# Kernel optimization log

Hardware: AMD Instinct MI355X
Metric: run time of the kernel (lower is better)

The kernel has to match this reference:

```python
import jax, jax.numpy as jnp
import numpy as np

H = 128          # num_hidden
NUM_IN = 256     # 2*H: h_E (H) + gathered neighbor h_V (H)
SCALE = 30.0
LN_EPS = 1e-5


def _ln(x, g, b):
    mu = jnp.mean(x, axis=-1, keepdims=True)
    var = jnp.mean((x - mu) ** 2, axis=-1, keepdims=True)
    return (x - mu) * jax.lax.rsqrt(var + LN_EPS) * g + b


def _gather_nodes(nodes, idx):
    # nodes: [B,L,C], idx: [B,L,K] -> [B,L,K,C]
    B = nodes.shape[0]
    return nodes[jnp.arange(B)[:, None, None], idx]


def _mlp3(x, W1, b1, W2, b2, W3, b3):
    h = jax.nn.gelu(x @ W1 + b1, approximate=False)
    h = jax.nn.gelu(h @ W2 + b2, approximate=False)
    return h @ W3 + b3


def setup_inputs() -> dict:
    key = jax.random.key(0)
    ks = jax.random.split(key, 16)
    B, L, K = 2, 2048, 48
    s = 0.02
    inp = {
        "h_V": jax.random.normal(ks[0], (B, L, H), jnp.float32),
        "h_E": jax.random.normal(ks[1], (B, L, K, H), jnp.float32),
        "E_idx": jax.random.randint(ks[2], (B, L, K), 0, L, jnp.int32),
        "mask_V": jnp.ones((B, L), jnp.float32),
        "mask_attend": jnp.ones((B, L, K), jnp.float32),
        # node-update MLP
        "W1": jax.random.normal(ks[3], (H + NUM_IN, H), jnp.float32) * s,
        "b1": jnp.zeros((H,), jnp.float32),
        "W2": jax.random.normal(ks[4], (H, H), jnp.float32) * s,
        "b2": jnp.zeros((H,), jnp.float32),
        "W3": jax.random.normal(ks[5], (H, H), jnp.float32) * s,
        "b3": jnp.zeros((H,), jnp.float32),
        # edge-update MLP
        "W11": jax.random.normal(ks[6], (H + NUM_IN, H), jnp.float32) * s,
        "b11": jnp.zeros((H,), jnp.float32),
        "W12": jax.random.normal(ks[7], (H, H), jnp.float32) * s,
        "b12": jnp.zeros((H,), jnp.float32),
        "W13": jax.random.normal(ks[8], (H, H), jnp.float32) * s,
        "b13": jnp.zeros((H,), jnp.float32),
        # position-wise FFN (H -> 4H -> H)
        "Win": jax.random.normal(ks[9], (H, 4 * H), jnp.float32) * s,
        "bin": jnp.zeros((4 * H,), jnp.float32),
        "Wout": jax.random.normal(ks[10], (4 * H, H), jnp.float32) * s,
        "bout": jnp.zeros((H,), jnp.float32),
        # LayerNorms
        "g1": jnp.ones((H,), jnp.float32), "be1": jnp.zeros((H,), jnp.float32),
        "g2": jnp.ones((H,), jnp.float32), "be2": jnp.zeros((H,), jnp.float32),
        "g3": jnp.ones((H,), jnp.float32), "be3": jnp.zeros((H,), jnp.float32),
    }
    return inp


def reference(h_V, h_E, E_idx, mask_V, mask_attend,
              W1, b1, W2, b2, W3, b3,
              W11, b11, W12, b12, W13, b13,
              Win, bin, Wout, bout,
              g1, be1, g2, be2, g3, be3):
    K = h_E.shape[-2]
    # --- node update: gather, concat, 3-layer MLP, masked mean-sum, LN residual ---
    h_nbr = _gather_nodes(h_V, E_idx)                               # [B,L,K,H]
    h_V_exp = jnp.broadcast_to(h_V[:, :, None, :], h_nbr.shape)     # [B,L,K,H]
    h_EV = jnp.concatenate([h_V_exp, h_E, h_nbr], axis=-1)          # [B,L,K,3H]
    h_msg = _mlp3(h_EV, W1, b1, W2, b2, W3, b3)                     # [B,L,K,H]
    h_msg = mask_attend[..., None] * h_msg
    dh = jnp.sum(h_msg, axis=-2) / SCALE                            # [B,L,H]
    h_V = _ln(h_V + dh, g1, be1)
    # position-wise FFN + LN residual
    dh = jax.nn.gelu(h_V @ Win + bin, approximate=False) @ Wout + bout
    h_V = _ln(h_V + dh, g2, be2)
    h_V = mask_V[..., None] * h_V
    # --- edge update ---
    h_nbr = _gather_nodes(h_V, E_idx)
    h_V_exp = jnp.broadcast_to(h_V[:, :, None, :], h_nbr.shape)
    h_EV = jnp.concatenate([h_V_exp, h_E, h_nbr], axis=-1)
    h_msg = _mlp3(h_EV, W11, b11, W12, b12, W13, b13)
    h_E = _ln(h_E + h_msg, g3, be3)
    return (h_V, h_E)
```

## Files before the change

kernel.cpp:

```cpp
#include <hip/hip_runtime.h>
#include <hip/hip_bf16.h>

typedef __attribute__((ext_vector_type(8))) short short8;
typedef __attribute__((ext_vector_type(4))) float f32x4;

__device__ inline short f2bf(float f) {
    unsigned u = __builtin_bit_cast(unsigned, f);
    u += 0x7fffu + ((u >> 16) & 1u);
    return (short)(u >> 16);
}
__device__ inline float bf2f(short s) {
    return __builtin_bit_cast(float, ((unsigned)(unsigned short)s) << 16);
}
__device__ inline unsigned cvt_pk_bf16(float a, float b) {
    unsigned r;
    asm("v_cvt_pk_bf16_f32 %0, %1, %2" : "=v"(r) : "v"(a), "v"(b));
    return r;
}
__device__ inline float gelu_fast(float x) {
    float z = x * (1.0f + 0.044715f * x * x);
    float e = __expf(1.5957691216f * z);
    return x - x * __builtin_amdgcn_rcpf(e + 1.0f);
}
__device__ inline float wred(float s) {
#pragma unroll
    for (int o = 32; o; o >>= 1) s += __shfl_xor(s, o, 64);
    return s;
}

__global__ void pack_all_kernel(const float* __restrict__ W1, const float* __restrict__ W2,
                                const float* __restrict__ W3, const float* __restrict__ W11,
                                const float* __restrict__ W12, const float* __restrict__ W13,
                                const float* __restrict__ Win, const float* __restrict__ Wout,
                                short* __restrict__ out) {
    int b = blockIdx.x;
    if (b < 80) {
        int which = b >> 3;
        const float* Ws[10] = {W1 + 128 * 128, W2, W3, W11 + 128 * 128, W12, W13,
                               W1, W1 + 256 * 128, W11, W11 + 256 * 128};
        const float* W = Ws[which];
        int i = (b & 7) * 256 + threadIdx.x;
        int lane = i & 63, tile = i >> 6;
        int kt = tile & 3, nt = tile >> 2;
        int n = nt * 16 + (lane & 15);
        int k0 = kt * 32 + (lane >> 4) * 8;
        short8 v;
#pragma unroll
        for (int j = 0; j < 8; ++j) v[j] = f2bf(W[(size_t)(k0 + j) * 128 + n]);
        *(short8*)(out + (size_t)which * 16384 + (size_t)i * 8) = v;
    } else if (b < 112) {
        int i = (b - 80) * 256 + threadIdx.x;
        int lane = i & 63, tile = i >> 6;
        int kt = tile & 3, nt = tile >> 2;
        int n = nt * 16 + (lane & 15);
        int k0 = kt * 32 + (lane >> 4) * 8;
        short8 v;
#pragma unroll
        for (int j = 0; j < 8; ++j) v[j] = f2bf(Win[(size_t)(k0 + j) * 512 + n]);
        *(short8*)(out + 163840 + (size_t)i * 8) = v;
    } else {
        int i = (b - 112) * 256 + threadIdx.x;
        int lane = i & 63, tile = i >> 6;
        int kt = tile & 15, nt = tile >> 4;
        int n = nt * 16 + (lane & 15);
        int k0 = kt * 32 + (lane >> 4) * 8;
        short8 v;
#pragma unroll
        for (int j = 0; j < 8; ++j) v[j] = f2bf(Wout[(size_t)(k0 + j) * 128 + n]);
        *(short8*)(out + 229376 + (size_t)i * 8) = v;
    }
}

__global__ __launch_bounds__(256) void node_pre_kernel(
    const float* __restrict__ hV, const short8* __restrict__ Bs,
    const short8* __restrict__ Bn, const float* __restrict__ bias,
    float* __restrict__ Ys, short* __restrict__ Yn) {
    int n0 = blockIdx.x * 16;
    int tid = threadIdx.x, lane = tid & 63, w = tid >> 6;
    __shared__ __align__(16) short A_sw[16 * 128];
    {
        int off = tid * 8;
        int r = off >> 7, c0 = off & 127;
        const float* src = hV + (size_t)n0 * 128 + off;
        float4 f0 = *(const float4*)(src);
        float4 f1 = *(const float4*)(src + 4);
        uint4 u;
        u.x = cvt_pk_bf16(f0.x, f0.y); u.y = cvt_pk_bf16(f0.z, f0.w);
        u.z = cvt_pk_bf16(f1.x, f1.y); u.w = cvt_pk_bf16(f1.z, f1.w);
        *(uint4*)((char*)A_sw + r * 256 + ((c0 * 2) ^ ((r & 7) << 4))) = u;
    }
    __syncthreads();
    const short8* Bp = (w < 2) ? Bs : Bn;
    f32x4 acc[4];
#pragma unroll
    for (int n2 = 0; n2 < 4; ++n2) acc[n2] = (f32x4){0.f, 0.f, 0.f, 0.f};
#pragma unroll
    for (int kt = 0; kt < 4; ++kt) {
        int row = lane & 15;
        int kb = (kt * 32 + (lane >> 4) * 8) * 2;
        short8 a = *(const short8*)((const char*)A_sw + row * 256 + (kb ^ ((row & 7) << 4)));
#pragma unroll
        for (int n2 = 0; n2 < 4; ++n2) {
            int ntl = (w & 1) * 4 + n2;
            short8 bf = Bp[(ntl * 4 + kt) * 64 + lane];
            acc[n2] = __builtin_amdgcn_mfma_f32_16x16x32_bf16(a, bf, acc[n2], 0, 0, 0);
        }
    }
    if (w < 2) {
#pragma unroll
        for (int n2 = 0; n2 < 4; ++n2) {
            int col = ((w & 1) * 4 + n2) * 16 + (lane & 15);
            float bv = bias[col];
#pragma unroll
            for (int i = 0; i < 4; ++i) {
                int row = (lane >> 4) * 4 + i;
                Ys[(size_t)(n0 + row) * 128 + col] = acc[n2][i] + bv;
            }
        }
    } else {
#pragma unroll
        for (int n2 = 0; n2 < 4; ++n2) {
            int col = ((w & 1) * 4 + n2) * 16 + (lane & 15);
#pragma unroll
            for (int i = 0; i < 4; ++i) {
                int row = (lane >> 4) * 4 + i;
                Yn[(size_t)(n0 + row) * 128 + col] = f2bf(acc[n2][i]);
            }
        }
    }
}


__device__ inline void gemm48_a(const short* A_sw, const short8* __restrict__ Wp,
                                int w, int lane, f32x4 acc[3][2]) {
#pragma unroll
    for (int mt = 0; mt < 3; ++mt)
#pragma unroll
        for (int n2 = 0; n2 < 2; ++n2) acc[mt][n2] = (f32x4){0.f, 0.f, 0.f, 0.f};
#pragma unroll
    for (int kt = 0; kt < 4; ++kt) {
        short8 a[3];
        int kb = (kt * 32 + (lane >> 4) * 8) * 2;
#pragma unroll
        for (int mt = 0; mt < 3; ++mt) {
            int row = mt * 16 + (lane & 15);
            a[mt] = *(const short8*)((const char*)A_sw + row * 256 + (kb ^ ((row & 7) << 4)));
        }
#pragma unroll
        for (int n2 = 0; n2 < 2; ++n2) {
            short8 bf = Wp[((w * 2 + n2) * 4 + kt) * 64 + lane];
#pragma unroll
            for (int mt = 0; mt < 3; ++mt)
                acc[mt][n2] = __builtin_amdgcn_mfma_f32_16x16x32_bf16(a[mt], bf, acc[mt][n2], 0, 0, 0);
        }
    }
}

__device__ inline void gemm48_swz(const short* A_sw, const short8* __restrict__ Wp,
                                  int w, int lane, f32x4 acc[2][3]) {
#pragma unroll
    for (int m2 = 0; m2 < 2; ++m2)
#pragma unroll
        for (int nt = 0; nt < 3; ++nt) acc[m2][nt] = (f32x4){0.f, 0.f, 0.f, 0.f};
#pragma unroll
    for (int kt = 0; kt < 4; ++kt) {
        int kb = (kt * 32 + (lane >> 4) * 8) * 2;
        short8 e[3];
#pragma unroll
        for (int nt = 0; nt < 3; ++nt) {
            int row = nt * 16 + (lane & 15);
            e[nt] = *(const short8*)((const char*)A_sw + row * 256 + (kb ^ ((row & 7) << 4)));
        }
#pragma unroll
        for (int m2 = 0; m2 < 2; ++m2) {
            short8 wf = Wp[((w * 2 + m2) * 4 + kt) * 64 + lane];
#pragma unroll
            for (int nt = 0; nt < 3; ++nt)
                acc[m2][nt] = __builtin_amdgcn_mfma_f32_16x16x32_bf16(wf, e[nt], acc[m2][nt], 0, 0, 0);
        }
    }
}

__device__ inline void stage_hE(const float* __restrict__ Eb, short* A_sw, int tid) {
#pragma unroll
    for (int i = 0; i < 3; ++i) {
        int e = tid + i * 256;
        int r = e >> 4, c0 = (e & 15) * 8;
        float4 f0 = *(const float4*)(Eb + r * 128 + c0);
        float4 f1 = *(const float4*)(Eb + r * 128 + c0 + 4);
        uint4 u;
        u.x = cvt_pk_bf16(f0.x, f0.y); u.y = cvt_pk_bf16(f0.z, f0.w);
        u.z = cvt_pk_bf16(f1.x, f1.y); u.w = cvt_pk_bf16(f1.z, f1.w);
        *(uint4*)((char*)A_sw + r * 256 + ((c0 * 2) ^ ((r & 7) << 4))) = u;
    }
}

__device__ inline void gather_Yn(const short* __restrict__ Yng, const int* __restrict__ Eidx,
                                 int node, int bb, int tid, short* Ygb) {
    if (tid < 192) {
        int r = tid >> 2, q = tid & 3;
        int idx = Eidx[node * 48 + r];
        const short8* src = (const short8*)(Yng + ((size_t)bb * 2048 + idx) * 128 + q * 32);
        short8* dst = (short8*)(Ygb + r * 136 + q * 32);
        dst[0] = src[0];
        dst[1] = src[1];
        dst[2] = src[2];
        dst[3] = src[3];
    }
}

__device__ inline void epi_l1(f32x4 acc[2][3], const float* Ysh, const short* Ygb,
                              short* A_sw, int w, int lane) {
#pragma unroll
    for (int m2 = 0; m2 < 2; ++m2) {
        int featb = (w * 2 + m2) * 16 + ((lane >> 4) << 2);
        float ys0 = Ysh[featb], ys1 = Ysh[featb + 1];
        float ys2 = Ysh[featb + 2], ys3 = Ysh[featb + 3];
#pragma unroll
        for (int nt = 0; nt < 3; ++nt) {
            int edge = nt * 16 + (lane & 15);
            uint2 yv = *(const uint2*)(Ygb + edge * 136 + featb);
            float v0 = gelu_fast(acc[m2][nt][0] + ys0 + __builtin_bit_cast(float, yv.x << 16));
            float v1 = gelu_fast(acc[m2][nt][1] + ys1 + __builtin_bit_cast(float, yv.x & 0xffff0000u));
            float v2 = gelu_fast(acc[m2][nt][2] + ys2 + __builtin_bit_cast(float, yv.y << 16));
            float v3 = gelu_fast(acc[m2][nt][3] + ys3 + __builtin_bit_cast(float, yv.y & 0xffff0000u));
            uint2 pk = {cvt_pk_bf16(v0, v1), cvt_pk_bf16(v2, v3)};
            *(uint2*)((char*)A_sw + edge * 256 + ((featb * 2) ^ ((edge & 7) << 4))) = pk;
        }
    }
}

__device__ inline void epi_l2(f32x4 acc[2][3], const float* __restrict__ b,
                              short* A_sw, int w, int lane) {
#pragma unroll
    for (int m2 = 0; m2 < 2; ++m2) {
        int featb = (w * 2 + m2) * 16 + ((lane >> 4) << 2);
        float b0 = b[featb], b1 = b[featb + 1], b2v = b[featb + 2], b3v = b[featb + 3];
#pragma unroll
        for (int nt = 0; nt < 3; ++nt) {
            int edge = nt * 16 + (lane & 15);
            float v0 = gelu_fast(acc[m2][nt][0] + b0);
            float v1 = gelu_fast(acc[m2][nt][1] + b1);
            float v2 = gelu_fast(acc[m2][nt][2] + b2v);
            float v3 = gelu_fast(acc[m2][nt][3] + b3v);
            uint2 pk = {cvt_pk_bf16(v0, v1), cvt_pk_bf16(v2, v3)};
            *(uint2*)((char*)A_sw + edge * 256 + ((featb * 2) ^ ((edge & 7) << 4))) = pk;
        }
    }
}

__global__ __launch_bounds__(256) void node_msg_kernel(
    const float* __restrict__ hV, const float* __restrict__ hE,
    const int* __restrict__ Eidx, const float* __restrict__ maskAtt,
    const short8* __restrict__ W1bp, const short8* __restrict__ W2p,
    const short8* __restrict__ W3p, const float* __restrict__ b2,
    const float* __restrict__ b3, const float* __restrict__ Ysg,
    const short* __restrict__ Yng, const float* __restrict__ g1,
    const float* __restrict__ be1, float* __restrict__ hv1out) {
    const int node = blockIdx.x;
    const int bb = node >> 11;
    const int tid = threadIdx.x;
    const int lane = tid & 63, w = tid >> 6;

    __shared__ __align__(16) short A_sw[48 * 128];
    __shared__ __align__(16) short Ygb[48 * 136];
    __shared__ float Ysh[128];
    __shared__ float mask_s[48];
    __shared__ float red[8];

    stage_hE(hE + (size_t)node * 6144, A_sw, tid);
    if (tid < 128) Ysh[tid] = Ysg[(size_t)node * 128 + tid];
    if (tid >= 128 && tid < 176) mask_s[tid - 128] = maskAtt[node * 48 + tid - 128];
    gather_Yn(Yng, Eidx, node, bb, tid, Ygb);
    __syncthreads();

    f32x4 acc[2][3];
    gemm48_swz(A_sw, W1bp, w, lane, acc);
    __syncthreads();
    epi_l1(acc, Ysh, Ygb, A_sw, w, lane);
    __syncthreads();
    gemm48_swz(A_sw, W2p, w, lane, acc);
    __syncthreads();
    epi_l2(acc, b2, A_sw, w, lane);
    __syncthreads();

    f32x4 acc3[3][2];
    gemm48_a(A_sw, W3p, w, lane, acc3);
    float u[2];
#pragma unroll
    for (int n2 = 0; n2 < 2; ++n2) {
        int col = (w * 2 + n2) * 16 + (lane & 15);
        float b3c = b3[col];
        float s = 0.f;
#pragma unroll
        for (int mt = 0; mt < 3; ++mt)
#pragma unroll
            for (int i = 0; i < 4; ++i) {
                int row = mt * 16 + (lane >> 4) * 4 + i;
                s += (acc3[mt][n2][i] + b3c) * mask_s[row];
            }
        s += __shfl_xor(s, 16, 64);
        s += __shfl_xor(s, 32, 64);
        u[n2] = hV[(size_t)node * 128 + col] + s * (1.0f / 30.0f);
    }
    float ps = wred(u[0] + u[1]) * 0.25f;
    float pq = wred(u[0] * u[0] + u[1] * u[1]) * 0.25f;
    if (lane == 0) { red[w] = ps; red[4 + w] = pq; }
    __syncthreads();
    float S = red[0] + red[1] + red[2] + red[3];
    float Q = red[4] + red[5] + red[6] + red[7];
    float mu = S * (1.0f / 128.0f);
    float var = Q * (1.0f / 128.0f) - mu * mu;
    float rs = rsqrtf(var + 1e-5f);
    if ((lane >> 4) == 0) {
#pragma unroll
        for (int n2 = 0; n2 < 2; ++n2) {
            int col = (w * 2 + n2) * 16 + (lane & 15);
            hv1out[(size_t)node * 128 + col] = (u[n2] - mu) * rs * g1[col] + be1[col];
        }
    }
}

__global__ __launch_bounds__(256) void ffn_kernel(
    const float* __restrict__ hv1, const short8* __restrict__ Winp,
    const float* __restrict__ binp, const short8* __restrict__ Woutp,
    const float* __restrict__ bout, const float* __restrict__ g2,
    const float* __restrict__ be2, const float* __restrict__ maskV,
    float* __restrict__ hVout) {
    int n0 = blockIdx.x * 16;
    int tid = threadIdx.x, lane = tid & 63, w = tid >> 6;
    __shared__ float X[16 * 128];
    __shared__ __align__(16) short A_sw[16 * 128];
    __shared__ __align__(16) short H_sw[16 * 512];

    {
        int off = tid * 8;
        int r = off >> 7, c0 = off & 127;
        const float* src = hv1 + (size_t)n0 * 128 + off;
        float4 f0 = *(const float4*)(src);
        float4 f1 = *(const float4*)(src + 4);
        *(float4*)(&X[off]) = f0;
        *(float4*)(&X[off + 4]) = f1;
        uint4 u;
        u.x = cvt_pk_bf16(f0.x, f0.y); u.y = cvt_pk_bf16(f0.z, f0.w);
        u.z = cvt_pk_bf16(f1.x, f1.y); u.w = cvt_pk_bf16(f1.z, f1.w);
        *(uint4*)((char*)A_sw + r * 256 + ((c0 * 2) ^ ((r & 7) << 4))) = u;
    }
    __syncthreads();

    f32x4 acc1[8];
#pragma unroll
    for (int n2 = 0; n2 < 8; ++n2) acc1[n2] = (f32x4){0.f, 0.f, 0.f, 0.f};
#pragma unroll
    for (int kt = 0; kt < 4; ++kt) {
        int row = lane & 15;
        int kb = (kt * 32 + (lane >> 4) * 8) * 2;
        short8 a = *(const short8*)((const char*)A_sw + row * 256 + (kb ^ ((row & 7) << 4)));
#pragma unroll
        for (int n2 = 0; n2 < 8; ++n2) {
            short8 bf = Winp[((w * 8 + n2) * 4 + kt) * 64 + lane];
            acc1[n2] = __builtin_amdgcn_mfma_f32_16x16x32_bf16(a, bf, acc1[n2], 0, 0, 0);
        }
    }
#pragma unroll
    for (int n2 = 0; n2 < 8; ++n2) {
        int col = (w * 8 + n2) * 16 + (lane & 15);
        float bv = binp[col];
#pragma unroll
        for (int i = 0; i < 4; ++i) {
            int row = (lane >> 4) * 4 + i;
            float v = gelu_fast(acc1[n2][i] + bv);
            *(short*)((char*)H_sw + row * 1024 + ((col * 2) ^ ((row & 7) << 4))) = f2bf(v);
        }
    }
    __syncthreads();

    f32x4 acc2[2];
    acc2[0] = (f32x4){0.f, 0.f, 0.f, 0.f};
    acc2[1] = (f32x4){0.f, 0.f, 0.f, 0.f};
#pragma unroll
    for (int kt = 0; kt < 16; ++kt) {
        int row = lane & 15;
        int kb = (kt * 32 + (lane >> 4) * 8) * 2;
        short8 a = *(const short8*)((const char*)H_sw + row * 1024 + (kb ^ ((row & 7) << 4)));
#pragma unroll
        for (int n2 = 0; n2 < 2; ++n2) {
            short8 bf = Woutp[((w * 2 + n2) * 16 + kt) * 64 + lane];
            acc2[n2] = __builtin_amdgcn_mfma_f32_16x16x32_bf16(a, bf, acc2[n2], 0, 0, 0);
        }
    }
#pragma unroll
    for (int n2 = 0; n2 < 2; ++n2) {
        int col = (w * 2 + n2) * 16 + (lane & 15);
        float bo = bout[col];
#pragma unroll
        for (int i = 0; i < 4; ++i) {
            int row = (lane >> 4) * 4 + i;
            X[row * 128 + col] += acc2[n2][i] + bo;
        }
    }
    __syncthreads();

#pragma unroll
    for (int p = 0; p < 4; ++p) {
        int r = p * 4 + w;
        float u0 = X[r * 128 + lane], u1 = X[r * 128 + lane + 64];
        float s = wred(u0 + u1);
        float q = wred(u0 * u0 + u1 * u1);
        float mu = s * (1.0f / 128.0f);
        float var = q * (1.0f / 128.0f) - mu * mu;
        float rs = rsqrtf(var + 1e-5f);
        float mv = maskV[n0 + r];
        hVout[(size_t)(n0 + r) * 128 + lane] = mv * ((u0 - mu) * rs * g2[lane] + be2[lane]);
        hVout[(size_t)(n0 + r) * 128 + lane + 64] = mv * ((u1 - mu) * rs * g2[lane + 64] + be2[lane + 64]);
    }
}

__global__ __launch_bounds__(256) void edge_upd_kernel(
    const float* __restrict__ hE, const int* __restrict__ Eidx,
    const short8* __restrict__ W11bp, const short8* __restrict__ W12p,
    const short8* __restrict__ W13p, const float* __restrict__ b12,
    const float* __restrict__ b13, const float* __restrict__ Ysg,
    const short* __restrict__ Yng, const float* __restrict__ g3,
    const float* __restrict__ be3, float* __restrict__ hEout) {
    const int node = blockIdx.x;
    const int bb = node >> 11;
    const int tid = threadIdx.x;
    const int lane = tid & 63, w = tid >> 6;

    __shared__ __align__(16) short A_sw[48 * 128];
    __shared__ __align__(16) short Ygb[48 * 136];
    __shared__ float Ysh[128];

    const float* Eb = hE + (size_t)node * 6144;
    stage_hE(Eb, A_sw, tid);
    if (tid < 128) Ysh[tid] = Ysg[(size_t)node * 128 + tid];
    gather_Yn(Yng, Eidx, node, bb, tid, Ygb);
    __syncthreads();

    f32x4 acc[2][3];
    gemm48_swz(A_sw, W11bp, w, lane, acc);
    __syncthreads();
    epi_l1(acc, Ysh, Ygb, A_sw, w, lane);
    __syncthreads();
    gemm48_swz(A_sw, W12p, w, lane, acc);
    __syncthreads();
    epi_l2(acc, b12, A_sw, w, lane);
    __syncthreads();

    f32x4 acc3[3][2];
    gemm48_a(A_sw, W13p, w, lane, acc3);
#pragma unroll
    for (int mt = 0; mt < 3; ++mt)
#pragma unroll
        for (int n2 = 0; n2 < 2; ++n2) {
            int col = (w * 2 + n2) * 16 + (lane & 15);
            float bv = b13[col];
#pragma unroll
            for (int i = 0; i < 4; ++i) {
                int row = mt * 16 + (lane >> 4) * 4 + i;
                float v = acc3[mt][n2][i] + bv + Eb[row * 128 + col];
                Ygb[row * 136 + col] = f2bf(v);
            }
        }
    __syncthreads();

    float* outb = hEout + (size_t)node * 6144;
    float gl0 = g3[lane], gl1 = g3[lane + 64];
    float bl0 = be3[lane], bl1 = be3[lane + 64];
#pragma unroll
    for (int p = 0; p < 12; ++p) {
        int r = p * 4 + w;
        float u0 = bf2f(Ygb[r * 136 + lane]);
        float u1 = bf2f(Ygb[r * 136 + lane + 64]);
        float s = wred(u0 + u1);
        float q = wred(u0 * u0 + u1 * u1);
        float mu = s * (1.0f / 128.0f);
        float var = q * (1.0f / 128.0f) - mu * mu;
        float rs = rsqrtf(var + 1e-5f);
        outb[r * 128 + lane] = (u0 - mu) * rs * gl0 + bl0;
        outb[r * 128 + lane + 64] = (u1 - mu) * rs * gl1 + bl1;
    }
}

extern "C" void kernel_launch(void* const* d_in, const int* in_sizes, int n_in,
                              void* d_out, int out_size, void* d_ws, size_t ws_size,
                              hipStream_t stream) {
    const float* hV      = (const float*)d_in[0];
    const float* hE      = (const float*)d_in[1];
    const int*   Eidx    = (const int*)d_in[2];
    const float* maskV   = (const float*)d_in[3];
    const float* maskAtt = (const float*)d_in[4];
    const float* W1  = (const float*)d_in[5];
    const float* b1  = (const float*)d_in[6];
    const float* W2  = (const float*)d_in[7];
    const float* b2  = (const float*)d_in[8];
    const float* W3  = (const float*)d_in[9];
    const float* b3  = (const float*)d_in[10];
    const float* W11 = (const float*)d_in[11];
    const float* b11 = (const float*)d_in[12];
    const float* W12 = (const float*)d_in[13];
    const float* b12 = (const float*)d_in[14];
    const float* W13 = (const float*)d_in[15];
    const float* b13 = (const float*)d_in[16];
    const float* Win = (const float*)d_in[17];
    const float* binp= (const float*)d_in[18];
    const float* Wout= (const float*)d_in[19];
    const float* bout= (const float*)d_in[20];
    const float* g1  = (const float*)d_in[21];
    const float* be1 = (const float*)d_in[22];
    const float* g2  = (const float*)d_in[23];
    const float* be2 = (const float*)d_in[24];
    const float* g3  = (const float*)d_in[25];
    const float* be3 = (const float*)d_in[26];

    char* ws = (char*)d_ws;
    short* Wpk  = (short*)ws;
    float* Ys   = (float*)(ws + 1048576);
    short* Yn   = (short*)(ws + 1048576 + 2097152);
    float* hv1  = (float*)(ws + 1048576 + 2097152 + 1048576);

    float* hVout = (float*)d_out;
    float* hEout = hVout + 2 * 2048 * 128;

    const int NNODE = 2 * 2048;

    pack_all_kernel<<<144, 256, 0, stream>>>(W1, W2, W3, W11, W12, W13, Win, Wout, Wpk);

    node_pre_kernel<<<NNODE / 16, 256, 0, stream>>>(hV,
        (const short8*)(Wpk + 98304), (const short8*)(Wpk + 114688), b1, Ys, Yn);

    node_msg_kernel<<<NNODE, 256, 0, stream>>>(hV, hE, Eidx, maskAtt,
        (const short8*)(Wpk), (const short8*)(Wpk + 16384), (const short8*)(Wpk + 32768),
        b2, b3, Ys, Yn, g1, be1, hv1);

    ffn_kernel<<<NNODE / 16, 256, 0, stream>>>(hv1,
        (const short8*)(Wpk + 163840), binp, (const short8*)(Wpk + 229376), bout,
        g2, be2, maskV, hVout);

    node_pre_kernel<<<NNODE / 16, 256, 0, stream>>>(hVout,
        (const short8*)(Wpk + 131072), (const short8*)(Wpk + 147456), b11, Ys, Yn);

    edge_upd_kernel<<<NNODE, 256, 0, stream>>>(hE, Eidx,
        (const short8*)(Wpk + 49152), (const short8*)(Wpk + 65536), (const short8*)(Wpk + 81920),
        b12, b13, Ys, Yn, g3, be3, hEout);
}
```

Measured before the change: 134.9 us.

## Load gathered neighbor and self terms straight into registers, skip LDS staging

```diff
diff --git a/kernel.cpp b/kernel.cpp
--- a/kernel.cpp
+++ b/kernel.cpp
@@ -12,6 +12,8 @@
 __device__ inline float bf2f(short s) {
     return __builtin_bit_cast(float, ((unsigned)(unsigned short)s) << 16);
 }
+__device__ inline float bflo(unsigned u) { return __builtin_bit_cast(float, u << 16); }
+__device__ inline float bfhi(unsigned u) { return __builtin_bit_cast(float, u & 0xffff0000u); }
 __device__ inline unsigned cvt_pk_bf16(float a, float b) {
     unsigned r;
     asm("v_cvt_pk_bf16_f32 %0, %1, %2" : "=v"(r) : "v"(a), "v"(b));
@@ -195,35 +197,19 @@
     }
 }
 
-__device__ inline void gather_Yn(const short* __restrict__ Yng, const int* __restrict__ Eidx,
-                                 int node, int bb, int tid, short* Ygb) {
-    if (tid < 192) {
-        int r = tid >> 2, q = tid & 3;
-        int idx = Eidx[node * 48 + r];
-        const short8* src = (const short8*)(Yng + ((size_t)bb * 2048 + idx) * 128 + q * 32);
-        short8* dst = (short8*)(Ygb + r * 136 + q * 32);
-        dst[0] = src[0];
-        dst[1] = src[1];
-        dst[2] = src[2];
-        dst[3] = src[3];
-    }
-}
-
-__device__ inline void epi_l1(f32x4 acc[2][3], const float* Ysh, const short* Ygb,
-                              short* A_sw, int w, int lane) {
+__device__ inline void epi_l1_reg(f32x4 acc[2][3], const float4 ysv[2],
+                                  const uint2 ynv[3][2], short* A_sw, int w, int lane) {
 #pragma unroll
     for (int m2 = 0; m2 < 2; ++m2) {
         int featb = (w * 2 + m2) * 16 + ((lane >> 4) << 2);
-        float ys0 = Ysh[featb], ys1 = Ysh[featb + 1];
-        float ys2 = Ysh[featb + 2], ys3 = Ysh[featb + 3];
 #pragma unroll
         for (int nt = 0; nt < 3; ++nt) {
             int edge = nt * 16 + (lane & 15);
-            uint2 yv = *(const uint2*)(Ygb + edge * 136 + featb);
-            float v0 = gelu_fast(acc[m2][nt][0] + ys0 + __builtin_bit_cast(float, yv.x << 16));
-            float v1 = gelu_fast(acc[m2][nt][1] + ys1 + __builtin_bit_cast(float, yv.x & 0xffff0000u));
-            float v2 = gelu_fast(acc[m2][nt][2] + ys2 + __builtin_bit_cast(float, yv.y << 16));
-            float v3 = gelu_fast(acc[m2][nt][3] + ys3 + __builtin_bit_cast(float, yv.y & 0xffff0000u));
+            uint2 yv = ynv[nt][m2];
+            float v0 = gelu_fast(acc[m2][nt][0] + ysv[m2].x + bflo(yv.x));
+            float v1 = gelu_fast(acc[m2][nt][1] + ysv[m2].y + bfhi(yv.x));
+            float v2 = gelu_fast(acc[m2][nt][2] + ysv[m2].z + bflo(yv.y));
+            float v3 = gelu_fast(acc[m2][nt][3] + ysv[m2].w + bfhi(yv.y));
             uint2 pk = {cvt_pk_bf16(v0, v1), cvt_pk_bf16(v2, v3)};
             *(uint2*)((char*)A_sw + edge * 256 + ((featb * 2) ^ ((edge & 7) << 4))) = pk;
         }
@@ -263,21 +249,35 @@
     const int lane = tid & 63, w = tid >> 6;
 
     __shared__ __align__(16) short A_sw[48 * 128];
-    __shared__ __align__(16) short Ygb[48 * 136];
-    __shared__ float Ysh[128];
     __shared__ float mask_s[48];
     __shared__ float red[8];
 
+    const int e0 = lane & 15;
+    int featb0 = (w * 2) * 16 + ((lane >> 4) << 2);
+    int featb1 = featb0 + 16;
+    uint2 ynv[3][2];
+    float4 ysv[2];
+    {
+        int i0 = Eidx[node * 48 + e0];
+        int i1 = Eidx[node * 48 + 16 + e0];
+        int i2 = Eidx[node * 48 + 32 + e0];
+        const short* Y0 = Yng + ((size_t)bb * 2048 + i0) * 128;
+        const short* Y1 = Yng + ((size_t)bb * 2048 + i1) * 128;
+        const short* Y2 = Yng + ((size_t)bb * 2048 + i2) * 128;
+        ynv[0][0] = *(const uint2*)(Y0 + featb0); ynv[0][1] = *(const uint2*)(Y0 + featb1);
+        ynv[1][0] = *(const uint2*)(Y1 + featb0); ynv[1][1] = *(const uint2*)(Y1 + featb1);
+        ynv[2][0] = *(const uint2*)(Y2 + featb0); ynv[2][1] = *(const uint2*)(Y2 + featb1);
+        ysv[0] = *(const float4*)(Ysg + (size_t)node * 128 + featb0);
+        ysv[1] = *(const float4*)(Ysg + (size_t)node * 128 + featb1);
+    }
     stage_hE(hE + (size_t)node * 6144, A_sw, tid);
-    if (tid < 128) Ysh[tid] = Ysg[(size_t)node * 128 + tid];
-    if (tid >= 128 && tid < 176) mask_s[tid - 128] = maskAtt[node * 48 + tid - 128];
-    gather_Yn(Yng, Eidx, node, bb, tid, Ygb);
+    if (tid < 48) mask_s[tid] = maskAtt[node * 48 + tid];
     __syncthreads();
 
     f32x4 acc[2][3];
     gemm48_swz(A_sw, W1bp, w, lane, acc);
     __syncthreads();
-    epi_l1(acc, Ysh, Ygb, A_sw, w, lane);
+    epi_l1_reg(acc, ysv, ynv, A_sw, w, lane);
     __syncthreads();
     gemm48_swz(A_sw, W2p, w, lane, acc);
     __syncthreads();
@@ -429,40 +429,65 @@
     const int lane = tid & 63, w = tid >> 6;
 
     __shared__ __align__(16) short A_sw[48 * 128];
-    __shared__ __align__(16) short Ygb[48 * 136];
-    __shared__ float Ysh[128];
+    __shared__ __align__(16) short Stash[48 * 136];
 
     const float* Eb = hE + (size_t)node * 6144;
+    const int e0 = lane & 15;
+    int featb0 = (w * 2) * 16 + ((lane >> 4) << 2);
+    int featb1 = featb0 + 16;
+    uint2 ynv[3][2];
+    float4 ysv[2];
+    {
+        int i0 = Eidx[node * 48 + e0];
+        int i1 = Eidx[node * 48 + 16 + e0];
+        int i2 = Eidx[node * 48 + 32 + e0];
+        const short* Y0 = Yng + ((size_t)bb * 2048 + i0) * 128;
+        const short* Y1 = Yng + ((size_t)bb * 2048 + i1) * 128;
+        const short* Y2 = Yng + ((size_t)bb * 2048 + i2) * 128;
+        ynv[0][0] = *(const uint2*)(Y0 + featb0); ynv[0][1] = *(const uint2*)(Y0 + featb1);
+        ynv[1][0] = *(const uint2*)(Y1 + featb0); ynv[1][1] = *(const uint2*)(Y1 + featb1);
+        ynv[2][0] = *(const uint2*)(Y2 + featb0); ynv[2][1] = *(const uint2*)(Y2 + featb1);
+        ysv[0] = *(const float4*)(Ysg + (size_t)node * 128 + featb0);
+        ysv[1] = *(const float4*)(Ysg + (size_t)node * 128 + featb1);
+    }
     stage_hE(Eb, A_sw, tid);
-    if (tid < 128) Ysh[tid] = Ysg[(size_t)node * 128 + tid];
-    gather_Yn(Yng, Eidx, node, bb, tid, Ygb);
     __syncthreads();
 
     f32x4 acc[2][3];
     gemm48_swz(A_sw, W11bp, w, lane, acc);
     __syncthreads();
-    epi_l1(acc, Ysh, Ygb, A_sw, w, lane);
+    epi_l1_reg(acc, ysv, ynv, A_sw, w, lane);
     __syncthreads();
     gemm48_swz(A_sw, W12p, w, lane, acc);
     __syncthreads();
+    float4 resv[3][2];
+#pragma unroll
+    for (int nt = 0; nt < 3; ++nt) {
+        int edge = nt * 16 + e0;
+        resv[nt][0] = *(const float4*)(Eb + edge * 128 + featb0);
+        resv[nt][1] = *(const float4*)(Eb + edge * 128 + featb1);
+    }
+    float4 b13v0 = *(const float4*)(b13 + featb0);
+    float4 b13v1 = *(const float4*)(b13 + featb1);
     epi_l2(acc, b12, A_sw, w, lane);
     __syncthreads();
 
-    f32x4 acc3[3][2];
-    gemm48_a(A_sw, W13p, w, lane, acc3);
-#pragma unroll
-    for (int mt = 0; mt < 3; ++mt)
-#pragma unroll
-        for (int n2 = 0; n2 < 2; ++n2) {
-            int col = (w * 2 + n2) * 16 + (lane & 15);
-            float bv = b13[col];
-#pragma unroll
-            for (int i = 0; i < 4; ++i) {
-                int row = mt * 16 + (lane >> 4) * 4 + i;
-                float v = acc3[mt][n2][i] + bv + Eb[row * 128 + col];
-                Ygb[row * 136 + col] = f2bf(v);
-            }
-        }
+    gemm48_swz(A_sw, W13p, w, lane, acc);
+#pragma unroll
+    for (int m2 = 0; m2 < 2; ++m2) {
+        float4 bv = m2 ? b13v1 : b13v0;
+        int featb = m2 ? featb1 : featb0;
+#pragma unroll
+        for (int nt = 0; nt < 3; ++nt) {
+            int edge = nt * 16 + e0;
+            float v0 = acc[m2][nt][0] + bv.x + resv[nt][m2].x;
+            float v1 = acc[m2][nt][1] + bv.y + resv[nt][m2].y;
+            float v2 = acc[m2][nt][2] + bv.z + resv[nt][m2].z;
+            float v3 = acc[m2][nt][3] + bv.w + resv[nt][m2].w;
+            uint2 pk = {cvt_pk_bf16(v0, v1), cvt_pk_bf16(v2, v3)};
+            *(uint2*)(Stash + edge * 136 + featb) = pk;
+        }
+    }
     __syncthreads();
 
     float* outb = hEout + (size_t)node * 6144;
@@ -471,8 +496,8 @@
 #pragma unroll
     for (int p = 0; p < 12; ++p) {
         int r = p * 4 + w;
-        float u0 = bf2f(Ygb[r * 136 + lane]);
-        float u1 = bf2f(Ygb[r * 136 + lane + 64]);
+        float u0 = bf2f(Stash[r * 136 + lane]);
+        float u1 = bf2f(Stash[r * 136 + lane + 64]);
         float s = wred(u0 + u1);
         float q = wred(u0 * u0 + u1 * u1);
         float mu = s * (1.0f / 128.0f);
```

Measured after the change: 141.6 us. 5.0% more time.
